# Performance work log

Measured on AMD Instinct MI355X. Metric: run time of the kernel, lower is better.

The kernel has to match this reference:

```python
import jax, jax.numpy as jnp
import numpy as np

B, H, L, E, M = 16, 8, 4096, 64, 64


def setup_inputs() -> dict:
    key = jax.random.key(0)
    k1, k2, k3 = jax.random.split(key, 3)
    x = jax.random.normal(k1, (B, H, L, E), dtype=jnp.float32)
    # nn.Parameter(torch.randn(E, E, M, 2) / sqrt(E))
    weights = jax.random.normal(k2, (E, E, M, 2), dtype=jnp.float32) / np.float32(np.sqrt(E))
    # torch.randperm(L//2)[:M].sort()[0] -> sorted unique mode indices in [0, L//2)
    index = jnp.sort(jax.random.permutation(k3, L // 2)[:M]).astype(jnp.int32)
    return {"x": x, "weights": weights, "index": index}


def reference(x, weights, index):
    Bx, Hx, Lx, Ex = x.shape
    xt = jnp.swapaxes(x, -1, -2)                      # [B,H,E,L]
    x_ft = jnp.fft.rfft(xt, axis=-1)                  # [B,H,E,L//2+1] complex64
    w_c = jax.lax.complex(weights[..., 0], weights[..., 1])  # [E,E,M] complex
    sel = x_ft[..., index]                            # gather K modes: [B,H,E,M]
    out_sel = jnp.einsum('bhei,eoi->bhoi', sel, w_c)  # per-mode complex matmul
    out_ft = jnp.zeros_like(x_ft).at[..., index].set(out_sel)  # scatter back
    out = jnp.fft.irfft(out_ft, n=Lx, axis=-1)        # [B,H,E,L] real
    return jnp.swapaxes(out, -1, -2)                  # [B,H,L,E]
```

## Files before the change

### kernel.cpp

```cpp
#include <hip/hip_runtime.h>

using half8 = __attribute__((ext_vector_type(8))) _Float16;
using f32x4 = __attribute__((ext_vector_type(4))) float;

#define Lc 4096
#define Ec 64
#define Mc 64
#define BHc 128
#define NCH 4
#define CHUNK (Lc / NCH)

#define TWO_PI_OVER_L 1.5339807878856412e-3f

__global__ __launch_bounds__(256) void twid_k(const int* __restrict__ idx,
                                              _Float16* __restrict__ Tt,
                                              _Float16* __restrict__ UL) {
    int id = blockIdx.x * 256 + threadIdx.x;
    {
        int l = id >> 7, m2 = id & 127, m = m2 & 63;
        int k = idx[m];
        int ph = (k * l) & (Lc - 1);
        float s, c;
        sincosf((float)ph * TWO_PI_OVER_L, &s, &c);
        UL[id] = (_Float16)((m2 >= 64) ? s : c);
    }
    {
        int m2 = id >> 12, l = id & 4095, m = m2 & 63;
        int k = idx[m];
        int ph = (k * l) & (Lc - 1);
        float s, c;
        sincosf((float)ph * TWO_PI_OVER_L, &s, &c);
        Tt[id] = (_Float16)((m2 >= 64) ? -s : c);
    }
}

__global__ __launch_bounds__(256) void fwd_k(const float* __restrict__ x,
                                             const _Float16* __restrict__ Tt,
                                             float* __restrict__ selP) {
    __shared__ _Float16 xs[Ec * 48];
    int bh = blockIdx.x, ch = blockIdx.y;
    int tid = threadIdx.x;
    int lane = tid & 63, w = tid >> 6;
    int eg = tid & 15, lp = tid >> 4;
    int lo16 = lane & 15, kg = lane >> 4;
    const float* xp = x + ((size_t)bh * Lc + (size_t)ch * CHUNK) * Ec;
    const _Float16* tp = Tt + (size_t)(w * 32 + lo16) * Lc + ch * CHUNK + kg * 8;
    f32x4 acc[2][4] = {};
    for (int s = 0; s < CHUNK / 32; ++s) {
        const float* gl = xp + (size_t)(s * 32 + 2 * lp) * Ec + eg * 4;
        float4 xa = *(const float4*)gl;
        float4 xb = *(const float4*)(gl + Ec);
        __syncthreads();
        {
            const float* pa = &xa.x;
            const float* pb = &xb.x;
            #pragma unroll
            for (int i = 0; i < 4; ++i) {
                unsigned short ua = __builtin_bit_cast(unsigned short, (_Float16)pa[i]);
                unsigned short ub = __builtin_bit_cast(unsigned short, (_Float16)pb[i]);
                unsigned int pk = ua | ((unsigned int)ub << 16);
                *(unsigned int*)&xs[(eg * 4 + i) * 48 + 2 * lp] = pk;
            }
        }
        __syncthreads();
        half8 A0 = *(const half8*)(tp + s * 32);
        half8 A1 = *(const half8*)(tp + 16 * Lc + s * 32);
        #pragma unroll
        for (int j = 0; j < 4; ++j) {
            half8 B = *(const half8*)&xs[(16 * j + lo16) * 48 + kg * 8];
            acc[0][j] = __builtin_amdgcn_mfma_f32_16x16x32_f16(A0, B, acc[0][j], 0, 0, 0);
            acc[1][j] = __builtin_amdgcn_mfma_f32_16x16x32_f16(A1, B, acc[1][j], 0, 0, 0);
        }
    }
    float* op = selP + (size_t)(ch * BHc + bh) * (128 * Ec);
    #pragma unroll
    for (int a = 0; a < 2; ++a)
        #pragma unroll
        for (int j = 0; j < 4; ++j)
            #pragma unroll
            for (int r = 0; r < 4; ++r) {
                int m2 = w * 32 + a * 16 + kg * 4 + r;
                int e  = 16 * j + lo16;
                op[m2 * Ec + e] = acc[a][j][r];
            }
}

__global__ __launch_bounds__(256) void mix_k(const float* __restrict__ selP,
                                             const float* __restrict__ wgt,
                                             const int* __restrict__ idx,
                                             _Float16* __restrict__ Vt) {
    __shared__ float sel_s[128 * 65];
    int bh = blockIdx.x, oh = blockIdx.y;
    int tid = threadIdx.x;
    #pragma unroll
    for (int i = 0; i < 8; ++i) {
        int f4 = i * 256 + tid;
        const float4* p0 = (const float4*)(selP + (size_t)(0 * BHc + bh) * 8192) + f4;
        const float4* p1 = (const float4*)(selP + (size_t)(1 * BHc + bh) * 8192) + f4;
        const float4* p2 = (const float4*)(selP + (size_t)(2 * BHc + bh) * 8192) + f4;
        const float4* p3 = (const float4*)(selP + (size_t)(3 * BHc + bh) * 8192) + f4;
        float4 a = *p0, b = *p1, c = *p2, d = *p3;
        int m2 = f4 >> 4, e4 = (f4 & 15) * 4;
        float* dst = &sel_s[m2 * 65 + e4];
        dst[0] = a.x + b.x + c.x + d.x;
        dst[1] = a.y + b.y + c.y + d.y;
        dst[2] = a.z + b.z + c.z + d.z;
        dst[3] = a.w + b.w + c.w + d.w;
    }
    __syncthreads();
    int og = tid & 7, mg = tid >> 3;
    int o0 = oh * 32 + og * 4;
    int m0 = mg * 2;
    float rR[4][2] = {{0}}, rI[4][2] = {{0}};
    for (int e = 0; e < Ec; ++e) {
        float sr0 = sel_s[m0 * 65 + e];
        float sr1 = sel_s[(m0 + 1) * 65 + e];
        float si0 = sel_s[(64 + m0) * 65 + e];
        float si1 = sel_s[(64 + m0 + 1) * 65 + e];
        #pragma unroll
        for (int i = 0; i < 4; ++i) {
            const float4* wp = (const float4*)&wgt[(((size_t)e * Ec + (o0 + i)) * Mc + m0) * 2];
            float4 wv = *wp;
            rR[i][0] += sr0 * wv.x - si0 * wv.y;
            rI[i][0] += sr0 * wv.y + si0 * wv.x;
            rR[i][1] += sr1 * wv.z - si1 * wv.w;
            rI[i][1] += sr1 * wv.w + si1 * wv.z;
        }
    }
    float s0 = (idx[m0] == 0 ? 1.0f : 2.0f) / (float)Lc;
    float s1 = (idx[m0 + 1] == 0 ? 1.0f : 2.0f) / (float)Lc;
    #pragma unroll
    for (int i = 0; i < 4; ++i) {
        _Float16* vp = Vt + ((size_t)bh * 64 + o0 + i) * 128;
        unsigned short r0 = __builtin_bit_cast(unsigned short, (_Float16)(rR[i][0] * s0));
        unsigned short r1 = __builtin_bit_cast(unsigned short, (_Float16)(rR[i][1] * s1));
        unsigned short i0 = __builtin_bit_cast(unsigned short, (_Float16)(-rI[i][0] * s0));
        unsigned short i1 = __builtin_bit_cast(unsigned short, (_Float16)(-rI[i][1] * s1));
        *(unsigned int*)&vp[m0]      = r0 | ((unsigned int)r1 << 16);
        *(unsigned int*)&vp[64 + m0] = i0 | ((unsigned int)i1 << 16);
    }
}

__global__ __launch_bounds__(256) void inv_k(const _Float16* __restrict__ UL,
                                             const _Float16* __restrict__ Vt,
                                             float* __restrict__ out) {
    __shared__ _Float16 vs[64 * 136];
    int bh = blockIdx.x, lb = blockIdx.y;
    int tid = threadIdx.x, lane = tid & 63, w = tid >> 6;
    int lo16 = lane & 15, kg = lane >> 4;
    #pragma unroll
    for (int i = 0; i < 4; ++i) {
        int f = i * 256 + tid;
        int row = f >> 4, seg = f & 15;
        uint4 t4 = *(const uint4*)(Vt + (size_t)bh * 8192 + row * 128 + seg * 8);
        *(uint4*)&vs[row * 136 + seg * 8] = t4;
    }
    __syncthreads();
    int lt0 = lb * 256 + w * 64;
    const _Float16* up = UL + (size_t)(lt0 + lo16) * 128 + kg * 8;
    f32x4 acc[4][4] = {};
    #pragma unroll
    for (int ks = 0; ks < 4; ++ks) {
        half8 Af[4];
        #pragma unroll
        for (int a = 0; a < 4; ++a)
            Af[a] = *(const half8*)(up + (size_t)a * 16 * 128 + ks * 32);
        #pragma unroll
        for (int j = 0; j < 4; ++j) {
            half8 Bf = *(const half8*)&vs[(16 * j + lo16) * 136 + ks * 32 + kg * 8];
            #pragma unroll
            for (int a = 0; a < 4; ++a)
                acc[a][j] = __builtin_amdgcn_mfma_f32_16x16x32_f16(Af[a], Bf, acc[a][j], 0, 0, 0);
        }
    }
    float* op = out + ((size_t)bh * Lc + lt0) * Ec;
    #pragma unroll
    for (int a = 0; a < 4; ++a)
        #pragma unroll
        for (int j = 0; j < 4; ++j)
            #pragma unroll
            for (int r = 0; r < 4; ++r) {
                int ll = a * 16 + kg * 4 + r;
                int o  = 16 * j + lo16;
                op[ll * Ec + o] = acc[a][j][r];
            }
}

extern "C" void kernel_launch(void* const* d_in, const int* in_sizes, int n_in,
                              void* d_out, int out_size, void* d_ws, size_t ws_size,
                              hipStream_t stream) {
    const float* x   = (const float*)d_in[0];
    const float* wgt = (const float*)d_in[1];
    const int*   idx = (const int*)d_in[2];
    float* out = (float*)d_out;

    char* ws = (char*)d_ws;
    float*    selP = (float*)ws;
    _Float16* Tt   = (_Float16*)(ws + (size_t)NCH * BHc * 8192 * 4);
    _Float16* UL   = Tt + (size_t)128 * Lc;
    _Float16* Vt   = UL + (size_t)Lc * 128;

    twid_k<<<2048, 256, 0, stream>>>(idx, Tt, UL);
    fwd_k<<<dim3(BHc, NCH), 256, 0, stream>>>(x, Tt, selP);
    mix_k<<<dim3(BHc, 2), 256, 0, stream>>>(selP, wgt, idx, Vt);
    inv_k<<<dim3(BHc, 16), 256, 0, stream>>>(UL, Vt, out);
}
```

Before: 131.5 us.

## Prefetch x tiles, swizzle LDS layout, and split forward DFT into more chunks

The forward projection kernel now processes 64-row tiles. It prefetches the next tile's x values into registers while the MFMAs run on the current one, and stores the fp16 tile in LDS with an XOR swizzle to avoid bank conflicts. When the workspace is large enough, the L dimension is split into 8 chunks instead of 4, doubling the grid to improve occupancy. The cost is more partial-sum traffic in selP, which the mixing kernel reduces over a runtime chunk count.

```diff
diff --git a/kernel.cpp b/kernel.cpp
--- a/kernel.cpp
+++ b/kernel.cpp
@@ -7,8 +7,6 @@
 #define Ec 64
 #define Mc 64
 #define BHc 128
-#define NCH 4
-#define CHUNK (Lc / NCH)
 
 #define TWO_PI_OVER_L 1.5339807878856412e-3f
 
@@ -34,42 +32,74 @@
     }
 }
 
+template<int NCH>
 __global__ __launch_bounds__(256) void fwd_k(const float* __restrict__ x,
                                              const _Float16* __restrict__ Tt,
                                              float* __restrict__ selP) {
-    __shared__ _Float16 xs[Ec * 48];
+    constexpr int CH = Lc / NCH;
+    constexpr int NT = CH / 64;
+    __shared__ _Float16 xs[64 * 64];
     int bh = blockIdx.x, ch = blockIdx.y;
     int tid = threadIdx.x;
     int lane = tid & 63, w = tid >> 6;
-    int eg = tid & 15, lp = tid >> 4;
     int lo16 = lane & 15, kg = lane >> 4;
-    const float* xp = x + ((size_t)bh * Lc + (size_t)ch * CHUNK) * Ec;
-    const _Float16* tp = Tt + (size_t)(w * 32 + lo16) * Lc + ch * CHUNK + kg * 8;
+    int col4 = tid & 15, lp = tid >> 4;
+
+    const float* xp = x + ((size_t)bh * Lc + (size_t)ch * CH) * Ec + col4 * 4;
+    const _Float16* tp = Tt + (size_t)(w * 32 + lo16) * Lc + ch * CH + kg * 8;
+
+    float4 xa[2], xb[2];
+    #pragma unroll
+    for (int i = 0; i < 2; ++i) {
+        const float* g = xp + (size_t)(2 * lp + 32 * i) * Ec;
+        xa[i] = *(const float4*)g;
+        xb[i] = *(const float4*)(g + Ec);
+    }
+
     f32x4 acc[2][4] = {};
-    for (int s = 0; s < CHUNK / 32; ++s) {
-        const float* gl = xp + (size_t)(s * 32 + 2 * lp) * Ec + eg * 4;
-        float4 xa = *(const float4*)gl;
-        float4 xb = *(const float4*)(gl + Ec);
+    for (int s = 0; s < NT; ++s) {
+        unsigned int pk[2][4];
+        #pragma unroll
+        for (int i = 0; i < 2; ++i) {
+            const float* pa = (const float*)&xa[i];
+            const float* pb = (const float*)&xb[i];
+            #pragma unroll
+            for (int j = 0; j < 4; ++j) {
+                unsigned short ua = __builtin_bit_cast(unsigned short, (_Float16)pa[j]);
+                unsigned short ub = __builtin_bit_cast(unsigned short, (_Float16)pb[j]);
+                pk[i][j] = ua | ((unsigned int)ub << 16);
+            }
+        }
         __syncthreads();
-        {
-            const float* pa = &xa.x;
-            const float* pb = &xb.x;
-            #pragma unroll
-            for (int i = 0; i < 4; ++i) {
-                unsigned short ua = __builtin_bit_cast(unsigned short, (_Float16)pa[i]);
-                unsigned short ub = __builtin_bit_cast(unsigned short, (_Float16)pb[i]);
-                unsigned int pk = ua | ((unsigned int)ub << 16);
-                *(unsigned int*)&xs[(eg * 4 + i) * 48 + 2 * lp] = pk;
-            }
-        }
+        #pragma unroll
+        for (int i = 0; i < 2; ++i)
+            #pragma unroll
+            for (int j = 0; j < 4; ++j) {
+                int jr = (j + col4) & 3;
+                int e = col4 * 4 + jr;
+                int byt = (e * 128 + lp * 4 + i * 64) ^ ((e & 7) << 4);
+                *(unsigned int*)((char*)xs + byt) = pk[i][jr];
+            }
         __syncthreads();
-        half8 A0 = *(const half8*)(tp + s * 32);
-        half8 A1 = *(const half8*)(tp + 16 * Lc + s * 32);
-        #pragma unroll
-        for (int j = 0; j < 4; ++j) {
-            half8 B = *(const half8*)&xs[(16 * j + lo16) * 48 + kg * 8];
-            acc[0][j] = __builtin_amdgcn_mfma_f32_16x16x32_f16(A0, B, acc[0][j], 0, 0, 0);
-            acc[1][j] = __builtin_amdgcn_mfma_f32_16x16x32_f16(A1, B, acc[1][j], 0, 0, 0);
+        if (s + 1 < NT) {
+            #pragma unroll
+            for (int i = 0; i < 2; ++i) {
+                const float* g = xp + (size_t)((s + 1) * 64 + 2 * lp + 32 * i) * Ec;
+                xa[i] = *(const float4*)g;
+                xb[i] = *(const float4*)(g + Ec);
+            }
+        }
+        #pragma unroll
+        for (int ks = 0; ks < 2; ++ks) {
+            half8 A0 = *(const half8*)(tp + s * 64 + ks * 32);
+            half8 A1 = *(const half8*)(tp + (size_t)16 * Lc + s * 64 + ks * 32);
+            #pragma unroll
+            for (int j = 0; j < 4; ++j) {
+                int rb = ((16 * j + lo16) * 128 + ks * 64 + kg * 16) ^ ((lo16 & 7) << 4);
+                half8 B = *(const half8*)((const char*)xs + rb);
+                acc[0][j] = __builtin_amdgcn_mfma_f32_16x16x32_f16(A0, B, acc[0][j], 0, 0, 0);
+                acc[1][j] = __builtin_amdgcn_mfma_f32_16x16x32_f16(A1, B, acc[1][j], 0, 0, 0);
+            }
         }
     }
     float* op = selP + (size_t)(ch * BHc + bh) * (128 * Ec);
@@ -88,24 +118,21 @@
 __global__ __launch_bounds__(256) void mix_k(const float* __restrict__ selP,
                                              const float* __restrict__ wgt,
                                              const int* __restrict__ idx,
-                                             _Float16* __restrict__ Vt) {
+                                             _Float16* __restrict__ Vt, int nch) {
     __shared__ float sel_s[128 * 65];
     int bh = blockIdx.x, oh = blockIdx.y;
     int tid = threadIdx.x;
     #pragma unroll
     for (int i = 0; i < 8; ++i) {
         int f4 = i * 256 + tid;
-        const float4* p0 = (const float4*)(selP + (size_t)(0 * BHc + bh) * 8192) + f4;
-        const float4* p1 = (const float4*)(selP + (size_t)(1 * BHc + bh) * 8192) + f4;
-        const float4* p2 = (const float4*)(selP + (size_t)(2 * BHc + bh) * 8192) + f4;
-        const float4* p3 = (const float4*)(selP + (size_t)(3 * BHc + bh) * 8192) + f4;
-        float4 a = *p0, b = *p1, c = *p2, d = *p3;
+        float4 a = make_float4(0.f, 0.f, 0.f, 0.f);
+        for (int chn = 0; chn < nch; ++chn) {
+            float4 v = *((const float4*)(selP + (size_t)(chn * BHc + bh) * 8192) + f4);
+            a.x += v.x; a.y += v.y; a.z += v.z; a.w += v.w;
+        }
         int m2 = f4 >> 4, e4 = (f4 & 15) * 4;
         float* dst = &sel_s[m2 * 65 + e4];
-        dst[0] = a.x + b.x + c.x + d.x;
-        dst[1] = a.y + b.y + c.y + d.y;
-        dst[2] = a.z + b.z + c.z + d.z;
-        dst[3] = a.w + b.w + c.w + d.w;
+        dst[0] = a.x; dst[1] = a.y; dst[2] = a.z; dst[3] = a.w;
     }
     __syncthreads();
     int og = tid & 7, mg = tid >> 3;
@@ -194,14 +221,20 @@
     const int*   idx = (const int*)d_in[2];
     float* out = (float*)d_out;
 
+    size_t need8 = (size_t)8 * BHc * 8192 * 4 + (2ull * 128 * Lc + (size_t)BHc * 8192) * 2;
+    int nch = (ws_size >= need8) ? 8 : 4;
+
     char* ws = (char*)d_ws;
     float*    selP = (float*)ws;
-    _Float16* Tt   = (_Float16*)(ws + (size_t)NCH * BHc * 8192 * 4);
+    _Float16* Tt   = (_Float16*)(ws + (size_t)nch * BHc * 8192 * 4);
     _Float16* UL   = Tt + (size_t)128 * Lc;
     _Float16* Vt   = UL + (size_t)Lc * 128;
 
     twid_k<<<2048, 256, 0, stream>>>(idx, Tt, UL);
-    fwd_k<<<dim3(BHc, NCH), 256, 0, stream>>>(x, Tt, selP);
-    mix_k<<<dim3(BHc, 2), 256, 0, stream>>>(selP, wgt, idx, Vt);
+    if (nch == 8)
+        fwd_k<8><<<dim3(BHc, 8), 256, 0, stream>>>(x, Tt, selP);
+    else
+        fwd_k<4><<<dim3(BHc, 4), 256, 0, stream>>>(x, Tt, selP);
+    mix_k<<<dim3(BHc, 2), 256, 0, stream>>>(selP, wgt, idx, Vt, nch);
     inv_k<<<dim3(BHc, 16), 256, 0, stream>>>(UL, Vt, out);
 }
```

After: 129.8 us. About the same (-1.4%).
